# Optimization experiments

Measured on AMD Instinct MI355X. Metric: run time of the kernel, lower is better.

## Reference

```python
import jax, jax.numpy as jnp
import numpy as np

HIDDEN = 1024
HEADS = 16
HEAD_DIM = HIDDEN // HEADS
SCALE = 1.0 / (HEAD_DIM ** 0.5)


def setup_inputs() -> dict:
    key = jax.random.key(0)
    k1, k2, k3 = jax.random.split(key, 3)
    B, S = 2, 2048
    x = jax.random.normal(k1, (B, S, HIDDEN), dtype=jnp.float32)
    # torch Linear weights: (out_features, in_features), y = x @ W.T
    qkv_w = jax.random.normal(k2, (3 * HIDDEN, HIDDEN), dtype=jnp.float32) * (HIDDEN ** -0.5)
    out_w = jax.random.normal(k3, (HIDDEN, HIDDEN), dtype=jnp.float32) * (HIDDEN ** -0.5)
    return {"x": x, "qkv_w": qkv_w, "out_w": out_w}


def reference(x, qkv_w, out_w):
    B, S, H = x.shape
    qkv = jnp.einsum('bsh,oh->bso', x, qkv_w)  # [B,S,3H]
    q, k, v = jnp.split(qkv, 3, axis=-1)
    def heads(t):
        return t.reshape(B, S, HEADS, HEAD_DIM).transpose(0, 2, 1, 3)  # [B,nh,S,hd]
    q, k, v = heads(q), heads(k), heads(v)
    scores = jnp.einsum('bhqd,bhkd->bhqk', q, k) * SCALE  # [B,nh,S,S]
    attn = jax.nn.softmax(scores, axis=-1)
    out = jnp.einsum('bhqk,bhkd->bhqd', attn, v)  # [B,nh,S,hd]
    out = out.transpose(0, 2, 1, 3).reshape(B, S, H)
    return jnp.einsum('bsh,oh->bso', out, out_w)
```

## Files before the change

### kernel.cpp

```cpp
#include <hip/hip_runtime.h>
#include <hip/hip_bf16.h>

#define BB 2
#define SS 2048
#define HH 1024
#define NH 16
#define HD 64
#define MM (BB * SS)
#define N_QKV (3 * HH)
#define KK HH

typedef __attribute__((ext_vector_type(8))) short short8;
typedef __attribute__((ext_vector_type(4))) float floatx4;
typedef __attribute__((ext_vector_type(16))) float floatx16;

#define MFMA16(a, b, c) __builtin_amdgcn_mfma_f32_16x16x32_bf16(a, b, c, 0, 0, 0)
#define MFMA32(a, b, c) __builtin_amdgcn_mfma_f32_32x32x16_bf16(a, b, c, 0, 0, 0)

__device__ __forceinline__ unsigned short f2bf(float f) {
  unsigned int u = __builtin_bit_cast(unsigned int, f);
  u += 0x7FFFu + ((u >> 16) & 1u);
  return (unsigned short)(u >> 16);
}

__device__ __forceinline__ float fexp2(float x) {
#if __has_builtin(__builtin_amdgcn_exp2f)
  return __builtin_amdgcn_exp2f(x);
#else
  float r; asm("v_exp_f32 %0, %1" : "=v"(r) : "v"(x)); return r;
#endif
}

__device__ __forceinline__ unsigned int pack2(float lo, float hi) {
  unsigned int a = __builtin_bit_cast(unsigned int, lo) + 0x8000u;
  unsigned int b = __builtin_bit_cast(unsigned int, hi) + 0x8000u;
  return __builtin_amdgcn_perm(b, a, 0x07060302u);
}

__device__ __forceinline__ void gl_lds16(const unsigned short* g, unsigned short* l) {
  __builtin_amdgcn_global_load_lds((const __attribute__((address_space(1))) void*)g,
                                   (__attribute__((address_space(3))) void*)l,
                                   16, 0, 0);
}

#define N4X (MM * HH / 4)
#define N4Q (N_QKV * KK / 4)
#define N4O (HH * KK / 4)
__global__ __launch_bounds__(256) void cast3_f32_bf16(const float* __restrict__ x,
                                                      const float* __restrict__ qw,
                                                      const float* __restrict__ ow,
                                                      unsigned short* __restrict__ xb,
                                                      unsigned short* __restrict__ qwb,
                                                      unsigned short* __restrict__ owb) {
  int i = blockIdx.x * blockDim.x + threadIdx.x;
  const float* src; unsigned short* dst; int idx;
  if (i < N4X) { src = x; dst = xb; idx = i; }
  else if (i < N4X + N4Q) { src = qw; dst = qwb; idx = i - N4X; }
  else { src = ow; dst = owb; idx = i - N4X - N4Q; }
  float4 f = ((const float4*)src)[idx];
  ushort4 u;
  u.x = f2bf(f.x); u.y = f2bf(f.y); u.z = f2bf(f.z); u.w = f2bf(f.w);
  ((ushort4*)dst)[idx] = u;
}

__global__ __launch_bounds__(256) void gemm_qkv(const unsigned short* __restrict__ A,
                                                const unsigned short* __restrict__ W,
                                                unsigned short* __restrict__ qb,
                                                unsigned short* __restrict__ kb,
                                                unsigned short* __restrict__ vtb) {
  __shared__ __attribute__((aligned(16))) unsigned short As[128 * 32];
  __shared__ __attribute__((aligned(16))) unsigned short Bs[128 * 32];
  const int tid = threadIdx.x;
  const int wave = tid >> 6, lane = tid & 63;
  const int quad = lane >> 4, lc = lane & 15;
  const int m0 = blockIdx.y * 128, n0 = blockIdx.x * 128;
  const int wm = (wave >> 1) * 64, wn = (wave & 1) * 64;

  floatx4 acc[4][4];
#pragma unroll
  for (int i = 0; i < 4; i++)
#pragma unroll
    for (int j = 0; j < 4; j++) acc[i][j] = (floatx4){0.f, 0.f, 0.f, 0.f};

  const unsigned short* Ag = A + (size_t)(m0 + (tid >> 2)) * KK + (tid & 3) * 8;
  const unsigned short* Bg = W + (size_t)(n0 + (tid >> 2)) * KK + (tid & 3) * 8;
  unsigned short* AsW = As + wave * 512;
  unsigned short* BsW = Bs + wave * 512;

  for (int k0 = 0; k0 < KK; k0 += 32) {
    gl_lds16(Ag + k0, AsW);
    gl_lds16(Ag + k0 + (size_t)64 * KK, AsW + 2048);
    gl_lds16(Bg + k0, BsW);
    gl_lds16(Bg + k0 + (size_t)64 * KK, BsW + 2048);
    __syncthreads();
    short8 af[4], bf[4];
#pragma unroll
    for (int i = 0; i < 4; i++) {
      af[i] = *(const short8*)(As + (wm + i * 16 + lc) * 32 + quad * 8);
      bf[i] = *(const short8*)(Bs + (wn + i * 16 + lc) * 32 + quad * 8);
    }
#pragma unroll
    for (int i = 0; i < 4; i++)
#pragma unroll
      for (int j = 0; j < 4; j++) acc[i][j] = MFMA16(af[i], bf[j], acc[i][j]);
    __syncthreads();
  }

  const float QSCALE = 0.125f * 1.44269504f;
#pragma unroll
  for (int j = 0; j < 4; j++) {
    int n = n0 + wn + j * 16 + lc;
#pragma unroll
    for (int i = 0; i < 4; i++) {
      int mbase = m0 + wm + i * 16 + quad * 4;
      int b = mbase >> 11;
      int s0 = mbase & 2047;
      if (n < HH) {
        int h = n >> 6, d = n & 63;
#pragma unroll
        for (int r = 0; r < 4; r++)
          qb[(((size_t)(b * NH + h) * SS + s0 + r) * HD) + d] = f2bf(acc[i][j][r] * QSCALE);
      } else if (n < 2 * HH) {
        int n2 = n - HH; int h = n2 >> 6, d = n2 & 63;
#pragma unroll
        for (int r = 0; r < 4; r++)
          kb[(((size_t)(b * NH + h) * SS + s0 + r) * HD) + d] = f2bf(acc[i][j][r]);
      } else {
        int n2 = n - 2 * HH; int h = n2 >> 6, d = n2 & 63;
        ushort4 p;
        p.x = f2bf(acc[i][j][0]); p.y = f2bf(acc[i][j][1]);
        p.z = f2bf(acc[i][j][2]); p.w = f2bf(acc[i][j][3]);
        *(ushort4*)(vtb + ((size_t)(b * NH + h) * HD + d) * SS + s0) = p;
      }
    }
  }
}

__device__ __forceinline__ int co(int row, int c16) {
  return row * 64 + ((c16 ^ ((row ^ (row >> 3)) & 7)) << 3);
}

__global__ __launch_bounds__(256, 2) void attn_kernel(const unsigned short* __restrict__ qg,
                                                      const unsigned short* __restrict__ kg,
                                                      const unsigned short* __restrict__ vtg,
                                                      unsigned short* __restrict__ og) {
  __shared__ __attribute__((aligned(16))) unsigned short Sall[16384];
  unsigned short* Qs = Sall;
  unsigned short* Ks = Sall + 8192;
  unsigned short* Vs = Sall + 12288;

  const int tid = threadIdx.x;
  const int w = tid >> 6, lane = tid & 63;
  const int hl = lane >> 5, c = lane & 31;
  const int q0 = blockIdx.x * 128;
  const int head = blockIdx.y, b = blockIdx.z;

  const unsigned short* qbase = qg + (size_t)(b * NH + head) * SS * HD;
  const unsigned short* kbase = kg + (size_t)(b * NH + head) * SS * HD;
  const unsigned short* vbase = vtg + (size_t)(b * NH + head) * HD * SS;

  {
    int row = tid >> 3, cc = tid & 7;
#pragma unroll
    for (int s = 0; s < 4; s++)
      *(uint4*)(Qs + co(row + 32 * s, cc)) =
          *(const uint4*)(qbase + (size_t)(q0 + row + 32 * s) * HD + cc * 8);
  }

  const int frow = tid >> 3, fc = tid & 7;
  uint4 k0r = *(const uint4*)(kbase + (size_t)frow * HD + fc * 8);
  uint4 k1r = *(const uint4*)(kbase + (size_t)(frow + 32) * HD + fc * 8);
  uint4 v0r = *(const uint4*)(vbase + (size_t)frow * SS + fc * 8);
  uint4 v1r = *(const uint4*)(vbase + (size_t)(frow + 32) * SS + fc * 8);

  floatx16 oacc0, oacc1, lacc;
#pragma unroll
  for (int i = 0; i < 16; i++) { oacc0[i] = 0.f; oacc1[i] = 0.f; lacc[i] = 0.f; }

  short8 ones;
#pragma unroll
  for (int i = 0; i < 8; i++) ones[i] = (short)0x3F80;

  short8 qa[4];

  for (int kt = 0; kt < SS; kt += 64) {
    __syncthreads();
    *(uint4*)(Ks + co(frow, fc)) = k0r;
    *(uint4*)(Ks + co(frow + 32, fc)) = k1r;
    *(uint4*)(Vs + co(frow, fc)) = v0r;
    *(uint4*)(Vs + co(frow + 32, fc)) = v1r;
    if (kt + 64 < SS) {
      k0r = *(const uint4*)(kbase + (size_t)(kt + 64 + frow) * HD + fc * 8);
      k1r = *(const uint4*)(kbase + (size_t)(kt + 96 + frow) * HD + fc * 8);
      v0r = *(const uint4*)(vbase + (size_t)frow * SS + kt + 64 + fc * 8);
      v1r = *(const uint4*)(vbase + (size_t)(frow + 32) * SS + kt + 64 + fc * 8);
    }
    __syncthreads();

    if (kt == 0) {
#pragma unroll
      for (int ks = 0; ks < 4; ks++)
        qa[ks] = *(const short8*)(Qs + co(w * 32 + c, ks * 2 + hl));
    }

    floatx16 sacc0, sacc1;
#pragma unroll
    for (int i = 0; i < 16; i++) { sacc0[i] = 0.f; sacc1[i] = 0.f; }
#pragma unroll
    for (int ks = 0; ks < 4; ks++) {
      short8 ka0 = *(const short8*)(Ks + co(c, ks * 2 + hl));
      short8 ka1 = *(const short8*)(Ks + co(32 + c, ks * 2 + hl));
      sacc0 = MFMA32(ka0, qa[ks], sacc0);
      sacc1 = MFMA32(ka1, qa[ks], sacc1);
    }

    short8 pb[4];
#pragma unroll
    for (int kb = 0; kb < 4; kb++) {
      const floatx16& s = (kb < 2) ? sacc0 : sacc1;
      int base = (kb & 1) * 8;
      unsigned int u0 = pack2(fexp2(s[base + 0]), fexp2(s[base + 1]));
      unsigned int u1 = pack2(fexp2(s[base + 2]), fexp2(s[base + 3]));
      unsigned int u2 = pack2(fexp2(s[base + 4]), fexp2(s[base + 5]));
      unsigned int u3 = pack2(fexp2(s[base + 6]), fexp2(s[base + 7]));
      uint4 u = {u0, u1, u2, u3};
      pb[kb] = __builtin_bit_cast(short8, u);
    }

#pragma unroll
    for (int kb = 0; kb < 4; kb++) {
      uint2 lo0 = *(const uint2*)(Vs + co(c, 2 * kb) + 4 * hl);
      uint2 hi0 = *(const uint2*)(Vs + co(c, 2 * kb + 1) + 4 * hl);
      uint4 a0 = {lo0.x, lo0.y, hi0.x, hi0.y};
      short8 va0 = __builtin_bit_cast(short8, a0);
      uint2 lo1 = *(const uint2*)(Vs + co(32 + c, 2 * kb) + 4 * hl);
      uint2 hi1 = *(const uint2*)(Vs + co(32 + c, 2 * kb + 1) + 4 * hl);
      uint4 a1 = {lo1.x, lo1.y, hi1.x, hi1.y};
      short8 va1 = __builtin_bit_cast(short8, a1);
      oacc0 = MFMA32(va0, pb[kb], oacc0);
      oacc1 = MFMA32(va1, pb[kb], oacc1);
      lacc = MFMA32(ones, pb[kb], lacc);
    }
  }

  __syncthreads();
  unsigned short* sc = Sall + w * 2176;
  float inv = 1.0f / lacc[0];
#pragma unroll
  for (int t = 0; t < 8; t++) {
    int d0 = ((2 * t) & 3) + 8 * (t >> 1) + 4 * hl;
    *(unsigned int*)(sc + c * 68 + d0) = pack2(oacc0[2 * t] * inv, oacc0[2 * t + 1] * inv);
    *(unsigned int*)(sc + c * 68 + 32 + d0) = pack2(oacc1[2 * t] * inv, oacc1[2 * t + 1] * inv);
  }
  {
    int ql = lane >> 1, hf = lane & 1;
    size_t row = (size_t)(b * SS + q0 + w * 32 + ql);
    unsigned short* dst = og + row * HH + head * 64 + hf * 32;
    const unsigned short* srcp = sc + ql * 68 + hf * 32;
#pragma unroll
    for (int s = 0; s < 4; s++) {
      uint2 a = *(const uint2*)(srcp + s * 8);
      uint2 bq = *(const uint2*)(srcp + s * 8 + 4);
      uint4 v = {a.x, a.y, bq.x, bq.y};
      *(uint4*)(dst + s * 8) = v;
    }
  }
}

__global__ __launch_bounds__(256) void gemm_out(const unsigned short* __restrict__ A,
                                                const unsigned short* __restrict__ W,
                                                float* __restrict__ C) {
  __shared__ __attribute__((aligned(16))) unsigned short As[128 * 32];
  __shared__ __attribute__((aligned(16))) unsigned short Bs[64 * 32];
  const int tid = threadIdx.x;
  const int wave = tid >> 6, lane = tid & 63;
  const int quad = lane >> 4, lc = lane & 15;
  const int m0 = blockIdx.y * 128, n0 = blockIdx.x * 64;
  const int wm = (wave >> 1) * 64, wn = (wave & 1) * 32;

  floatx4 acc[4][2];
#pragma unroll
  for (int i = 0; i < 4; i++)
#pragma unroll
    for (int j = 0; j < 2; j++) acc[i][j] = (floatx4){0.f, 0.f, 0.f, 0.f};

  const unsigned short* Ag = A + (size_t)(m0 + (tid >> 2)) * KK + (tid & 3) * 8;
  const unsigned short* Bg = W + (size_t)(n0 + (tid >> 2)) * KK + (tid & 3) * 8;

  for (int k0 = 0; k0 < KK; k0 += 32) {
    gl_lds16(Ag + k0, As + wave * 512);
    gl_lds16(Ag + k0 + (size_t)64 * KK, As + 2048 + wave * 512);
    gl_lds16(Bg + k0, Bs + wave * 512);
    __syncthreads();
    short8 af[4], bf[2];
#pragma unroll
    for (int i = 0; i < 4; i++)
      af[i] = *(const short8*)(As + (wm + i * 16 + lc) * 32 + quad * 8);
#pragma unroll
    for (int j = 0; j < 2; j++)
      bf[j] = *(const short8*)(Bs + (wn + j * 16 + lc) * 32 + quad * 8);
#pragma unroll
    for (int i = 0; i < 4; i++)
#pragma unroll
      for (int j = 0; j < 2; j++) acc[i][j] = MFMA16(af[i], bf[j], acc[i][j]);
    __syncthreads();
  }

#pragma unroll
  for (int i = 0; i < 4; i++)
#pragma unroll
    for (int j = 0; j < 2; j++) {
      int m = m0 + wm + i * 16 + quad * 4;
      int n = n0 + wn + j * 16 + lc;
#pragma unroll
      for (int r = 0; r < 4; r++) C[(size_t)(m + r) * HH + n] = acc[i][j][r];
    }
}

extern "C" void kernel_launch(void* const* d_in, const int* in_sizes, int n_in,
                              void* d_out, int out_size, void* d_ws, size_t ws_size,
                              hipStream_t stream) {
  const float* x = (const float*)d_in[0];
  const float* qkv_w = (const float*)d_in[1];
  const float* out_w = (const float*)d_in[2];
  float* out = (float*)d_out;

  char* ws = (char*)d_ws;
  unsigned short* x_bf   = (unsigned short*)(ws + 0);
  unsigned short* qkw_bf = (unsigned short*)(ws + 8388608);
  unsigned short* otw_bf = (unsigned short*)(ws + 14680064);
  unsigned short* qb     = (unsigned short*)(ws + 16777216);
  unsigned short* kb     = (unsigned short*)(ws + 25165824);
  unsigned short* vtb    = (unsigned short*)(ws + 33554432);
  unsigned short* ao     = (unsigned short*)(ws + 41943040);

  cast3_f32_bf16<<<dim3((N4X + N4Q + N4O) / 256), dim3(256), 0, stream>>>(
      x, qkv_w, out_w, x_bf, qkw_bf, otw_bf);
  gemm_qkv<<<dim3(N_QKV / 128, MM / 128), dim3(256), 0, stream>>>(x_bf, qkw_bf, qb, kb, vtb);
  attn_kernel<<<dim3(SS / 128, NH, BB), dim3(256), 0, stream>>>(qb, kb, vtb, ao);
  gemm_out<<<dim3(HH / 64, MM / 128), dim3(256), 0, stream>>>(ao, otw_bf, out);
}
```

Before: 193.3 us.

## Replace direct global-to-LDS loads with register-staged prefetch in projection GEMMs

```diff
diff --git a/kernel.cpp b/kernel.cpp
--- a/kernel.cpp
+++ b/kernel.cpp
@@ -35,12 +35,6 @@
   unsigned int a = __builtin_bit_cast(unsigned int, lo) + 0x8000u;
   unsigned int b = __builtin_bit_cast(unsigned int, hi) + 0x8000u;
   return __builtin_amdgcn_perm(b, a, 0x07060302u);
-}
-
-__device__ __forceinline__ void gl_lds16(const unsigned short* g, unsigned short* l) {
-  __builtin_amdgcn_global_load_lds((const __attribute__((address_space(1))) void*)g,
-                                   (__attribute__((address_space(3))) void*)l,
-                                   16, 0, 0);
 }
 
 #define N4X (MM * HH / 4)
@@ -84,14 +78,27 @@
 
   const unsigned short* Ag = A + (size_t)(m0 + (tid >> 2)) * KK + (tid & 3) * 8;
   const unsigned short* Bg = W + (size_t)(n0 + (tid >> 2)) * KK + (tid & 3) * 8;
-  unsigned short* AsW = As + wave * 512;
-  unsigned short* BsW = Bs + wave * 512;
-
-  for (int k0 = 0; k0 < KK; k0 += 32) {
-    gl_lds16(Ag + k0, AsW);
-    gl_lds16(Ag + k0 + (size_t)64 * KK, AsW + 2048);
-    gl_lds16(Bg + k0, BsW);
-    gl_lds16(Bg + k0 + (size_t)64 * KK, BsW + 2048);
+  unsigned short* AsW = As + wave * 512 + lane * 8;
+  unsigned short* BsW = Bs + wave * 512 + lane * 8;
+
+  uint4 a0 = *(const uint4*)(Ag);
+  uint4 a1 = *(const uint4*)(Ag + (size_t)64 * KK);
+  uint4 b0 = *(const uint4*)(Bg);
+  uint4 b1 = *(const uint4*)(Bg + (size_t)64 * KK);
+
+  for (int it = 0; it < KK / 32; ++it) {
+    __syncthreads();
+    *(uint4*)(AsW) = a0;
+    *(uint4*)(AsW + 2048) = a1;
+    *(uint4*)(BsW) = b0;
+    *(uint4*)(BsW + 2048) = b1;
+    if (it + 1 < KK / 32) {
+      int k0 = (it + 1) * 32;
+      a0 = *(const uint4*)(Ag + k0);
+      a1 = *(const uint4*)(Ag + k0 + (size_t)64 * KK);
+      b0 = *(const uint4*)(Bg + k0);
+      b1 = *(const uint4*)(Bg + k0 + (size_t)64 * KK);
+    }
     __syncthreads();
     short8 af[4], bf[4];
 #pragma unroll
@@ -103,7 +110,6 @@
     for (int i = 0; i < 4; i++)
 #pragma unroll
       for (int j = 0; j < 4; j++) acc[i][j] = MFMA16(af[i], bf[j], acc[i][j]);
-    __syncthreads();
   }
 
   const float QSCALE = 0.125f * 1.44269504f;
@@ -286,11 +292,24 @@
 
   const unsigned short* Ag = A + (size_t)(m0 + (tid >> 2)) * KK + (tid & 3) * 8;
   const unsigned short* Bg = W + (size_t)(n0 + (tid >> 2)) * KK + (tid & 3) * 8;
-
-  for (int k0 = 0; k0 < KK; k0 += 32) {
-    gl_lds16(Ag + k0, As + wave * 512);
-    gl_lds16(Ag + k0 + (size_t)64 * KK, As + 2048 + wave * 512);
-    gl_lds16(Bg + k0, Bs + wave * 512);
+  unsigned short* AsW = As + wave * 512 + lane * 8;
+  unsigned short* BsW = Bs + wave * 512 + lane * 8;
+
+  uint4 a0 = *(const uint4*)(Ag);
+  uint4 a1 = *(const uint4*)(Ag + (size_t)64 * KK);
+  uint4 b0 = *(const uint4*)(Bg);
+
+  for (int it = 0; it < KK / 32; ++it) {
+    __syncthreads();
+    *(uint4*)(AsW) = a0;
+    *(uint4*)(AsW + 2048) = a1;
+    *(uint4*)(BsW) = b0;
+    if (it + 1 < KK / 32) {
+      int k0 = (it + 1) * 32;
+      a0 = *(const uint4*)(Ag + k0);
+      a1 = *(const uint4*)(Ag + k0 + (size_t)64 * KK);
+      b0 = *(const uint4*)(Bg + k0);
+    }
     __syncthreads();
     short8 af[4], bf[2];
 #pragma unroll
@@ -303,7 +322,6 @@
     for (int i = 0; i < 4; i++)
 #pragma unroll
       for (int j = 0; j < 2; j++) acc[i][j] = MFMA16(af[i], bf[j], acc[i][j]);
-    __syncthreads();
   }
 
 #pragma unroll
```

Result: no change. 193.2 us (-0.0%).
